# Kernel optimization log

Hardware: AMD Instinct MI355X
Metric: run time of the kernel (lower is better)

Reference implementation:

```python
import jax, jax.numpy as jnp
import numpy as np

K = 5            # kernel_size per dim
KD = K ** 3      # 125 spline weight slots
DIM = 3
NUM_GRAPHS = 64
# (n_nodes, n_edges, c_in, c_mid, c_out) per pyramid level
LEVELS = [(20000, 320000, 1, 32, 64), (10000, 160000, 1, 64, 64),
          (5000, 80000, 1, 64, 64), (2500, 40000, 1, 64, 64), (1250, 20000, 1, 64, 64)]


def setup_inputs() -> dict:
    key = jax.random.key(0)
    inp = {}
    for i, (n, e, cin, c1, c2) in enumerate(LEVELS, start=1):
        ks = jax.random.split(jax.random.fold_in(key, i), 8)
        inp[f'x{i}'] = jax.random.normal(ks[0], (n, cin), jnp.float32)
        inp[f'pseudo{i}'] = jax.random.uniform(ks[1], (e, DIM), jnp.float32)  # in [0,1)
        inp[f'edge_index{i}'] = jax.random.randint(ks[2], (2, e), 0, n)
        inp[f'batch{i}'] = jnp.sort(jax.random.randint(ks[3], (n,), 0, NUM_GRAPHS))
        inp[f'W{i}a'] = 0.1 * jax.random.normal(ks[4], (KD, cin, c1), jnp.float32)
        inp[f'root{i}a'] = 0.1 * jax.random.normal(ks[5], (cin, c1), jnp.float32)
        inp[f'bias{i}a'] = jnp.zeros((c1,), jnp.float32)
        inp[f'W{i}b'] = 0.1 * jax.random.normal(ks[6], (KD, c1, c2), jnp.float32)
        inp[f'root{i}b'] = 0.1 * jax.random.normal(ks[7], (c1, c2), jnp.float32)
        inp[f'bias{i}b'] = jnp.zeros((c2,), jnp.float32)
    kf = jax.random.fold_in(key, 99)
    inp['fc_w'] = 0.05 * jax.random.normal(kf, (5 * 64, 10), jnp.float32)
    inp['fc_b'] = jnp.zeros((10,), jnp.float32)
    return inp


def _spline_conv(x, src, dst, pseudo, W, Wroot, bias):
    """Degree-1 open B-spline conv (torch_spline_conv), mean aggregation + root weight."""
    n, cin = x.shape
    v = pseudo * (K - 1)                       # [E,3], pseudo in [0,1)
    k0 = jnp.floor(v).astype(jnp.int32)        # lower knot index per dim
    frac = v - k0                              # fractional part per dim
    xs = x[src]                                # [E,cin] gather source feats
    # accumulate basis-weighted source features per (target node, kernel slot)
    acc = jnp.zeros((n, KD, cin), x.dtype)
    for bits in range(2 ** DIM):               # 8 corner combinations of linear spline
        w = jnp.ones((src.shape[0],), x.dtype)
        idx = jnp.zeros((src.shape[0],), jnp.int32)
        for d in range(DIM):
            b = (bits >> d) & 1
            w = w * (frac[:, d] if b else 1.0 - frac[:, d])
            idx = idx * K + (k0[:, d] + b)
        acc = acc.at[dst, idx].add(w[:, None] * xs)
    deg = jnp.zeros((n,), x.dtype).at[dst].add(1.0)
    out = jnp.einsum('nki,kio->no', acc, W) / jnp.maximum(deg, 1.0)[:, None]
    return out + x @ Wroot + bias


def _readout(f, batch):
    s = jax.ops.segment_sum(f, batch, num_segments=NUM_GRAPHS)
    cnt = jax.ops.segment_sum(jnp.ones((f.shape[0],), f.dtype), batch, num_segments=NUM_GRAPHS)
    return s / jnp.maximum(cnt, 1.0)[:, None]   # scatter_mean


def _level(x, ei, ps, bt, Wa, ra, ba, Wb, rb, bb):
    f = jax.nn.relu(_spline_conv(x, ei[0], ei[1], ps, Wa, ra, ba))
    f = jax.nn.relu(_spline_conv(f, ei[0], ei[1], ps, Wb, rb, bb))
    return _readout(f, bt)


def reference(x1, pseudo1, edge_index1, batch1, W1a, root1a, bias1a, W1b, root1b, bias1b,
              x2, pseudo2, edge_index2, batch2, W2a, root2a, bias2a, W2b, root2b, bias2b,
              x3, pseudo3, edge_index3, batch3, W3a, root3a, bias3a, W3b, root3b, bias3b,
              x4, pseudo4, edge_index4, batch4, W4a, root4a, bias4a, W4b, root4b, bias4b,
              x5, pseudo5, edge_index5, batch5, W5a, root5a, bias5a, W5b, root5b, bias5b,
              fc_w, fc_b):
    levels = [
        (x1, edge_index1, pseudo1, batch1, W1a, root1a, bias1a, W1b, root1b, bias1b),
        (x2, edge_index2, pseudo2, batch2, W2a, root2a, bias2a, W2b, root2b, bias2b),
        (x3, edge_index3, pseudo3, batch3, W3a, root3a, bias3a, W3b, root3b, bias3b),
        (x4, edge_index4, pseudo4, batch4, W4a, root4a, bias4a, W4b, root4b, bias4b),
        (x5, edge_index5, pseudo5, batch5, W5a, root5a, bias5a, W5b, root5b, bias5b),
    ]
    res = [_level(*lv) for lv in levels]
    h = jnp.concatenate(res, axis=1)            # [B,320]; eval mode -> dropout is identity
    logits = h @ fc_w + fc_b                    # [B,10]
    return jax.nn.log_softmax(logits, axis=1)
```

## Files before the change

### kernel.cpp

```cpp
#include <hip/hip_runtime.h>
#include <hip/hip_fp16.h>
#include <math.h>

#define NUM_GRAPHS 64

typedef unsigned short ushortT;
typedef __attribute__((ext_vector_type(8))) short bf16x8;
typedef __attribute__((ext_vector_type(4))) float f32x4;

constexpr int cN[5]       = {20000, 10000, 5000, 2500, 1250};
constexpr int cE[5]       = {320000, 160000, 80000, 40000, 20000};
constexpr int cNOFF[6]    = {0, 20000, 30000, 35000, 37500, 38750};
constexpr int cEOFF[6]    = {0, 320000, 480000, 560000, 600000, 620000};
constexpr int cEBLKOFF[6] = {0, 1250, 1875, 2188, 2345, 2424};
constexpr int cNBLKOFF[6] = {0, 79, 119, 139, 149, 154};
constexpr int cMT[5]      = {5064, 2564, 1314, 689, 377};
constexpr int cTILEOFF[6] = {0, 5064, 7628, 8942, 9631, 10008};
constexpr int cSEOFF[6]   = {0, 324096, 488192, 572288, 616384, 640512};
constexpr int cF1OFF[6]   = {0, 640000, 1280000, 1600000, 1760000, 1840000};
constexpr int cWOFF[6]    = {0, 32000, 96000, 160000, 224000, 288000};
constexpr int cABLK[6]    = {0, 1250, 1875, 2188, 2345, 2424};
constexpr int cRBOFF[5]   = {0, 256, 768, 1280, 1792};
constexpr int cWAOFF[6]   = {0, 512, 1536, 2560, 3584, 4608};
constexpr int cRGB[6]     = {0, 313, 470, 549, 589, 609};
constexpr int cPAIR[6]    = {0, 2532, 3814, 4471, 4816, 5005};

struct P5f { const float* p[5]; };
struct P5i { const int* p[5]; };

__device__ __forceinline__ int lvl_e(int b) {
    return (b >= cEBLKOFF[4]) ? 4 : (b >= cEBLKOFF[3]) ? 3 : (b >= cEBLKOFF[2]) ? 2 : (b >= cEBLKOFF[1]) ? 1 : 0;
}
__device__ __forceinline__ int lvl_n(int b) {
    return (b >= cNBLKOFF[4]) ? 4 : (b >= cNBLKOFF[3]) ? 3 : (b >= cNBLKOFF[2]) ? 2 : (b >= cNBLKOFF[1]) ? 1 : 0;
}

__device__ __forceinline__ ushortT f2bf(float f) {
    union { float f; unsigned int u; } v; v.f = f;
    unsigned int r = (v.u + 0x7FFFu + ((v.u >> 16) & 1u)) >> 16;
    return (ushortT)r;
}
__device__ __forceinline__ float h2f_lo(unsigned int u) {
    return __half2float(__ushort_as_half((ushortT)(u & 0xFFFFu)));
}
__device__ __forceinline__ float h2f_hi(unsigned int u) {
    return __half2float(__ushort_as_half((ushortT)(u >> 16)));
}

__global__ void k_hist(P5f PS, P5i EI, int* __restrict__ dcnt, int* __restrict__ bb) {
    int b = blockIdx.x;
    int l = lvl_e(b);
    int lb = b - cEBLKOFF[l];
    int E = cE[l];
    __shared__ int h[64];
    int t = threadIdx.x;
    if (t < 64) h[t] = 0;
    __syncthreads();
    int e = lb * 256 + t;
    if (e < E) {
        atomicAdd(&dcnt[cNOFF[l] + EI.p[l][E + e]], 1);
        const float* ps = PS.p[l];
        int c = (int)floorf(ps[e * 3] * 4.f) * 16 + (int)floorf(ps[e * 3 + 1] * 4.f) * 4
              + (int)floorf(ps[e * 3 + 2] * 4.f);
        atomicAdd(&h[c], 1);
    }
    __syncthreads();
    if (t < 64) bb[(size_t)b * 64 + t] = h[t];
}

__global__ void k_cellscan(int* __restrict__ bb_all, int* __restrict__ csPad,
                           int* __restrict__ cellTot, int* __restrict__ cot_all) {
    int l = blockIdx.x;
    int c = threadIdx.x;
    int* bb = bb_all + (size_t)cEBLKOFF[l] * 64;
    int nblk = cEBLKOFF[l + 1] - cEBLKOFF[l];
    int run = 0;
    int b = 0;
    for (; b + 16 <= nblk; b += 16) {
        int v[16];
#pragma unroll
        for (int u = 0; u < 16; u++) v[u] = bb[(b + u) * 64 + c];
#pragma unroll
        for (int u = 0; u < 16; u++) { bb[(b + u) * 64 + c] = run; run += v[u]; }
    }
    for (; b < nblk; b++) { int v = bb[b * 64 + c]; bb[b * 64 + c] = run; run += v; }
    int tot = run;
    cellTot[l * 64 + c] = tot;
    int tiles = (tot + 63) >> 6;
    int x = tiles;
#pragma unroll
    for (int off = 1; off < 64; off <<= 1) { int y = __shfl_up(x, off, 64); if (c >= off) x += y; }
    int tileBase = x - tiles;
    csPad[l * 64 + c] = tileBase * 64;
    int* cot = cot_all + cTILEOFF[l];
    for (int i = 0; i < tiles; i++) {
        int vv = tot - (i << 6); if (vv > 64) vv = 64;
        cot[tileBase + i] = c | (vv << 8);
    }
    int nT = __shfl(x, 63, 64);
    int mt = cMT[l];
    for (int i = nT + c; i < mt; i += 64) cot[i] = -1;
}

__global__ void k_nscan1(const int* __restrict__ dcnt, int* __restrict__ dbase, int* __restrict__ bsum) {
    int b = blockIdx.x;
    int l = lvl_n(b);
    int lb = b - cNBLKOFF[l];
    int n = cN[l];
    __shared__ int sh[256];
    int t = threadIdx.x;
    int i = lb * 256 + t;
    int v = (i < n) ? dcnt[cNOFF[l] + i] : 0;
    sh[t] = v;
    __syncthreads();
    for (int off = 1; off < 256; off <<= 1) {
        int y = (t >= off) ? sh[t - off] : 0;
        __syncthreads();
        sh[t] += y;
        __syncthreads();
    }
    if (i < n) dbase[cNOFF[l] + i] = sh[t] - v;
    if (t == 255) bsum[b] = sh[255];
}

__global__ void k_nscan2(const int* __restrict__ bsum, int* __restrict__ boff) {
    int l = blockIdx.x;
    int o = cNBLKOFF[l];
    int nb = cNBLKOFF[l + 1] - o;
    int t = threadIdx.x;
    int v = (t < nb) ? bsum[o + t] : 0;
    int s = v;
#pragma unroll
    for (int off = 1; off < 64; off <<= 1) { int y = __shfl_up(s, off, 64); if (t >= off) s += y; }
    int tot = __shfl(s, 63, 64);
    if (t < nb) boff[o + t] = s - v;
    int t2 = t + 64;
    int v2 = (t2 < nb) ? bsum[o + t2] : 0;
    int s2 = v2;
#pragma unroll
    for (int off = 1; off < 64; off <<= 1) { int y = __shfl_up(s2, off, 64); if (t >= off) s2 += y; }
    if (t2 < nb) boff[o + t2] = tot + s2 - v2;
}

__global__ void k_scatter(P5f PS, P5i EI, const int* __restrict__ bb, const int* __restrict__ csPad,
                          const int* __restrict__ dbase, const int* __restrict__ boff,
                          int* __restrict__ rank,
                          int4* __restrict__ cbrec, int4* __restrict__ darec,
                          int* __restrict__ cpos) {
    int b = blockIdx.x;
    int l = lvl_e(b);
    int lb = b - cEBLKOFF[l];
    int E = cE[l];
    __shared__ int base[64];
    __shared__ int cnt[64];
    int t = threadIdx.x;
    if (t < 64) { base[t] = bb[(size_t)b * 64 + t] + csPad[l * 64 + t]; cnt[t] = 0; }
    __syncthreads();
    int e = lb * 256 + t;
    if (e >= E) return;
    const float* ps = PS.p[l];
    float v0 = ps[e * 3] * 4.f, v1 = ps[e * 3 + 1] * 4.f, v2 = ps[e * 3 + 2] * 4.f;
    float f0 = floorf(v0), f1v = floorf(v1), f2v = floorf(v2);
    int c = (int)f0 * 16 + (int)f1v * 4 + (int)f2v;
    int r = atomicAdd(&cnt[c], 1);
    int posc = base[c] + r;
    const int* ei = EI.p[l];
    int src = ei[e];
    int dst = ei[E + e];
    int posd = dbase[cNOFF[l] + dst] + boff[cNBLKOFF[l] + (dst >> 8)]
             + atomicAdd(&rank[cNOFF[l] + dst], 1);
    unsigned int fxfy = (unsigned int)__half_as_ushort(__float2half(v0 - f0))
                      | ((unsigned int)__half_as_ushort(__float2half(v1 - f1v)) << 16);
    unsigned int fzp  = (unsigned int)__half_as_ushort(__float2half(v2 - f2v));
    int4 rc;
    rc.x = src; rc.y = 0; rc.z = (int)fxfy; rc.w = (int)fzp;
    cbrec[cSEOFF[l] + posc] = rc;
    int4 rd;
    rd.x = src | (dst << 16); rd.y = c; rd.z = (int)fxfy; rd.w = (int)fzp;
    darec[cEOFF[l] + posd] = rd;
    cpos[cEOFF[l] + posd] = posc;
}

__global__ void k_wswz(P5f WB, P5f RootB, P5f WA,
                       uint4* __restrict__ hi4, uint4* __restrict__ rb, uint4* __restrict__ wa) {
    int idx = blockIdx.x * 256 + threadIdx.x;
    if (idx >= 294912) return;
    if (idx < 288000) {
        int l = (idx >= 224000) ? 4 : (idx >= 160000) ? 3 : (idx >= 96000) ? 2 : (idx >= 32000) ? 1 : 0;
        int local = idx - cWOFF[l];
        int T = l ? 2 : 1, C = l ? 64 : 32;
        int lane = local & 63;
        int blk = (local >> 6) & 3;
        int rest = local >> 8;
        int st = rest % T, s = rest / T;
        int q = lane >> 4, n = blk * 16 + (lane & 15);
        const float* W = WB.p[l];
        union { ushortT u[8]; uint4 v; } ph;
#pragma unroll
        for (int j = 0; j < 8; j++) {
            int k = st * 32 + q * 8 + j;
            ph.u[j] = f2bf(W[((size_t)s * C + k) * 64 + n]);
        }
        hi4[idx] = ph.v;
    } else if (idx < 290304) {
        int id2 = idx - 288000;
        int l = (id2 >= 1792) ? 4 : (id2 >= 1280) ? 3 : (id2 >= 768) ? 2 : (id2 >= 256) ? 1 : 0;
        int local = id2 - cRBOFF[l];
        int lane = local & 63;
        int w = (local >> 6) & 3;
        int st = local >> 8;
        int q = lane >> 4, n = w * 16 + (lane & 15);
        const float* R = RootB.p[l];
        union { ushortT u[8]; uint4 v; } ph;
#pragma unroll
        for (int j = 0; j < 8; j++) {
            int k = st * 32 + q * 8 + j;
            ph.u[j] = f2bf(R[k * 64 + n]);
        }
        rb[id2] = ph.v;
    } else {
        int id3 = idx - 290304;
        int l = (id3 >= cWAOFF[4]) ? 4 : (id3 >= cWAOFF[3]) ? 3 : (id3 >= cWAOFF[2]) ? 2 : (id3 >= cWAOFF[1]) ? 1 : 0;
        int local = id3 - cWAOFF[l];
        int C1 = l ? 64 : 32;
        int numN = C1 / 16;
        int lane = local & 63;
        int rest = local >> 6;
        int nb = rest % numN, st = rest / numN;
        int q = lane >> 4, n = nb * 16 + (lane & 15);
        const float* Wsrc = WA.p[l];
        union { ushortT u[8]; uint4 v; } ph;
#pragma unroll
        for (int j = 0; j < 8; j++) {
            int k = st * 32 + q * 8 + j;
            ph.u[j] = (k < 125) ? f2bf(Wsrc[k * C1 + n]) : (ushortT)0;
        }
        wa[id3] = ph.v;
    }
}

__launch_bounds__(256)
__global__ void conv_a_fused(P5f X, P5f RootA, P5f BiasA,
                             const int4* __restrict__ darec, const uint4* __restrict__ wasw,
                             const int* __restrict__ dbase, const int* __restrict__ boff,
                             const int* __restrict__ dcnt, ushortT* __restrict__ f1bf) {
    __shared__ float S[16 * 126];
    __shared__ ushortT Sbf[16 * 136];
    __shared__ int infoS[256];
    __shared__ unsigned int fxyS[256];
    __shared__ unsigned int fzS[256];
    __shared__ float xsS[256];
    int b = blockIdx.x;
    int l = (b >= cABLK[4]) ? 4 : (b >= cABLK[3]) ? 3 : (b >= cABLK[2]) ? 2 : (b >= cABLK[1]) ? 1 : 0;
    int node0 = (b - cABLK[l]) * 16;
    int n = cN[l];
    int nn = n - node0; if (nn > 16) nn = 16;
    int t = threadIdx.x;
    for (int i = t; i < 16 * 126; i += 256) S[i] = 0.f;
    const int* db = dbase + cNOFF[l];
    const int* bo = boff + cNBLKOFF[l];
    int estart = db[node0] + bo[node0 >> 8];
    int vend = node0 + nn;
    int eend = (vend >= n) ? cE[l] : (db[vend] + bo[vend >> 8]);
    const float* x = X.p[l];
    const int4* dr = darec + cEOFF[l];
    const int bx = t & 1, by = (t >> 1) & 1, bz = (t >> 2) & 1;
    for (int cs = estart; cs < eend; cs += 256) {
        int p = cs + t;
        if (p < eend) {
            int4 r = dr[p];
            infoS[t] = ((((unsigned int)r.x) >> 16) - node0) * 64 + r.y;
            fxyS[t] = (unsigned int)r.z;
            fzS[t] = (unsigned int)r.w;
            xsS[t] = x[r.x & 0xFFFF];
        }
        __syncthreads();
        int ne = eend - cs; if (ne > 256) ne = 256;
        for (int j = (t >> 3); j < ne; j += 32) {
            int info = infoS[j];
            int nl = info >> 6, cell = info & 63;
            unsigned int uz = fxyS[j];
            float fx = h2f_lo(uz), fy = h2f_hi(uz), fz = h2f_lo(fzS[j]);
            float xs = xsS[j];
            int cx = cell >> 4, cy = (cell >> 2) & 3, cz = cell & 3;
            int slot = (cx + bx) * 25 + (cy + by) * 5 + (cz + bz);
            float wc = (bx ? fx : 1.f - fx) * (by ? fy : 1.f - fy) * (bz ? fz : 1.f - fz);
            atomicAdd(&S[nl * 126 + slot], wc * xs);
        }
        __syncthreads();
    }
    for (int i = t; i < 16 * 128; i += 256) {
        int node = i >> 7, k = i & 127;
        float v = (k < 126) ? S[node * 126 + k] : 0.f;
        Sbf[node * 136 + k] = f2bf(v);
    }
    __syncthreads();
    int lane = t & 63, w = t >> 6;
    int C1 = l ? 64 : 32;
    int numN = C1 >> 4;
    if (w < numN) {
        int q = lane >> 4, m = lane & 15;
        const uint4* wl = wasw + cWAOFF[l];
        f32x4 acc = (f32x4){0.f, 0.f, 0.f, 0.f};
#pragma unroll
        for (int st = 0; st < 4; st++) {
            bf16x8 a = *(const bf16x8*)&Sbf[m * 136 + st * 32 + q * 8];
            bf16x8 bw = __builtin_bit_cast(bf16x8, wl[(st * numN + w) * 64 + lane]);
            acc = __builtin_amdgcn_mfma_f32_16x16x32_bf16(a, bw, acc, 0, 0, 0);
        }
        int ch = w * 16 + m;
        float rv = RootA.p[l][ch], bv = BiasA.p[l][ch];
        const int* dcl = dcnt + cNOFF[l];
        ushortT* f1bfl = f1bf + cF1OFF[l];
#pragma unroll
        for (int rr = 0; rr < 4; rr++) {
            int row = q * 4 + rr;
            if (row < nn) {
                int gnode = node0 + row;
                int dv = dcl[gnode];
                float d = (float)(dv > 1 ? dv : 1);
                float o = acc[rr] / d + x[gnode] * rv + bv;
                f1bfl[(size_t)gnode * C1 + ch] = f2bf(fmaxf(o, 0.f));
            }
        }
    }
}

__launch_bounds__(256)
__global__ void k_rgemm(const ushortT* __restrict__ f1bf, const uint4* __restrict__ rb,
                        float* __restrict__ f2) {
    int b = blockIdx.x;
    int l = (b >= cRGB[4]) ? 4 : (b >= cRGB[3]) ? 3 : (b >= cRGB[2]) ? 2 : (b >= cRGB[1]) ? 1 : 0;
    int node0 = (b - cRGB[l]) * 64;
    int n = cN[l];
    int nn = n - node0; if (nn > 64) nn = 64;
    int t = threadIdx.x;
    int lane = t & 63, w = t >> 6;
    int q = lane >> 4, m = lane & 15;
    const int CIN = l ? 64 : 32;
    const int T = l ? 2 : 1;
    const ushortT* fl = f1bf + cF1OFF[l];
    const uint4* rbl = rb + cRBOFF[l];
    f32x4 C[4];
#pragma unroll
    for (int mt = 0; mt < 4; mt++) C[mt] = (f32x4){0.f, 0.f, 0.f, 0.f};
    for (int st = 0; st < T; st++) {
        bf16x8 bh = __builtin_bit_cast(bf16x8, rbl[(st * 4 + w) * 64 + lane]);
#pragma unroll
        for (int mt = 0; mt < 4; mt++) {
            int row = 16 * mt + m;
            int nr = node0 + row; if (nr > n - 1) nr = n - 1;
            bf16x8 a = *(const bf16x8*)&fl[(size_t)nr * CIN + st * 32 + q * 8];
            C[mt] = __builtin_amdgcn_mfma_f32_16x16x32_bf16(a, bh, C[mt], 0, 0, 0);
        }
    }
#pragma unroll
    for (int mt = 0; mt < 4; mt++)
#pragma unroll
        for (int rr = 0; rr < 4; rr++) {
            int row = 16 * mt + q * 4 + rr;
            if (row < nn)
                f2[(size_t)(cNOFF[l] + node0 + row) * 64 + 16 * w + m] = C[mt][rr];
        }
}

template<int CIN>
__device__ __forceinline__ void stage_issue(const ushortT* __restrict__ f1bfl, int srcx,
                                            ushortT* lregion, int lane) {
    const int NC = CIN / 8;
#pragma unroll
    for (int i = 0; i < NC; i++) {
        int s = i * 64 + lane;
        int row = s / NC;
        int cp = s & (NC - 1);
        int chunk = cp ^ (row & (NC - 1));
        int src = __shfl(srcx, row, 64);
        const ushortT* gp = f1bfl + (size_t)src * CIN + chunk * 8;
        __builtin_amdgcn_global_load_lds(
            (const __attribute__((address_space(1))) void*)gp,
            (__attribute__((address_space(3))) void*)(lregion + (size_t)i * 512),
            16, 0, 0);
    }
}

template<int CIN>
__device__ __forceinline__ void read_ahr(const ushortT* st, bf16x8 (&ahr)[4][CIN / 32],
                                         int q, int m) {
    const int NC = CIN / 8;
#pragma unroll
    for (int mt = 0; mt < 4; mt++) {
        int row = 16 * mt + m;
#pragma unroll
        for (int s = 0; s < CIN / 32; s++) {
            int chunk = s * 4 + q;
            int cp = chunk ^ (row & (NC - 1));
            ahr[mt][s] = *(const bf16x8*)&st[(size_t)row * NC * 8 + cp * 8];
        }
    }
}

template<int CIN>
__device__ __forceinline__ void conv_b_tile_compute(
    const uint4* __restrict__ whiL, __half* __restrict__ pout,
    bf16x8 (&ahr)[4][CIN / 32], const float* __restrict__ wxy,
    const float* __restrict__ fzp, int cell, int tb, int lane, int wv) {
    const int T = CIN / 32;
    int q = lane >> 4, m = lane & 15;
    int cx = cell >> 4, cy = (cell >> 2) & 3, cz = cell & 3;
    float fzr[16];
#pragma unroll
    for (int mt = 0; mt < 4; mt++)
#pragma unroll
        for (int rr = 0; rr < 4; rr++)
            fzr[mt * 4 + rr] = fzp[16 * mt + q * 4 + rr];

    uint4 wb[2][2 * T];
    auto loadw = [&](int xy, uint4* dst) {
        int bx = xy & 1, by = xy >> 1;
        int s0 = (cx + bx) * 25 + (cy + by) * 5 + cz;
#pragma unroll
        for (int st = 0; st < T; st++) {
            dst[st]     = whiL[((size_t)(s0 * T + st) * 4 + wv) * 64 + lane];
            dst[T + st] = whiL[((size_t)((s0 + 1) * T + st) * 4 + wv) * 64 + lane];
        }
    };
    loadw(0, wb[0]);

    f32x4 acc[4];
#pragma unroll
    for (int mt = 0; mt < 4; mt++) acc[mt] = (f32x4){0.f, 0.f, 0.f, 0.f};

#pragma unroll
    for (int xy = 0; xy < 4; xy++) {
        uint4* cur = wb[xy & 1];
        if (xy < 3) loadw(xy + 1, wb[(xy + 1) & 1]);
        f32x4 C0[4], C1[4];
#pragma unroll
        for (int mt = 0; mt < 4; mt++) {
            C0[mt] = (f32x4){0.f, 0.f, 0.f, 0.f};
            C1[mt] = (f32x4){0.f, 0.f, 0.f, 0.f};
        }
#pragma unroll
        for (int st = 0; st < T; st++) {
            bf16x8 b0 = __builtin_bit_cast(bf16x8, cur[st]);
            bf16x8 b1 = __builtin_bit_cast(bf16x8, cur[T + st]);
#pragma unroll
            for (int mt = 0; mt < 4; mt++) {
                C0[mt] = __builtin_amdgcn_mfma_f32_16x16x32_bf16(ahr[mt][st], b0, C0[mt], 0, 0, 0);
                C1[mt] = __builtin_amdgcn_mfma_f32_16x16x32_bf16(ahr[mt][st], b1, C1[mt], 0, 0, 0);
            }
        }
        const float* wrow = &wxy[xy * 64];
#pragma unroll
        for (int mt = 0; mt < 4; mt++)
#pragma unroll
            for (int rr = 0; rr < 4; rr++) {
                float wxyv = wrow[16 * mt + q * 4 + rr];
                float dlt = C1[mt][rr] - C0[mt][rr];
                float tt = fmaf(fzr[mt * 4 + rr], dlt, C0[mt][rr]);
                acc[mt][rr] = fmaf(wxyv, tt, acc[mt][rr]);
            }
    }
#pragma unroll
    for (int mt = 0; mt < 4; mt++)
#pragma unroll
        for (int rr = 0; rr < 4; rr++) {
            int row = 16 * mt + q * 4 + rr;
            pout[(size_t)(tb + row) * 64 + 16 * wv + m] = __float2half(acc[mt][rr]);
        }
}

template<int CIN>
__device__ __forceinline__ void conv_b_pair(
    const ushortT* __restrict__ f1bfl, const int4* __restrict__ cbl,
    const uint4* __restrict__ whiL, __half* __restrict__ pout,
    int d0, int d1, int tb0, int tb1, int lane, int wv,
    ushortT* stage0, ushortT* stage1,
    float* __restrict__ wxy0, float* __restrict__ fz0,
    float* __restrict__ wxy1, float* __restrict__ fz1) {
    const int T = CIN / 32;
    const int NC = CIN / 8;
    int q = lane >> 4, m = lane & 15;
    bool has1 = d1 >= 0;
    int cell0 = d0 & 63, v0 = d0 >> 8;
    int cell1 = has1 ? (d1 & 63) : 0, v1 = has1 ? (d1 >> 8) : 0;

    int4 r0, r1;
    if (lane < v0) r0 = cbl[tb0 + lane]; else { r0.x = 0; r0.y = 0; r0.z = 0; r0.w = 0; }
    if (lane < v1) r1 = cbl[tb1 + lane]; else { r1.x = 0; r1.y = 0; r1.z = 0; r1.w = 0; }

    {
        unsigned int uz = (unsigned int)r0.z;
        float fx = h2f_lo(uz), fy = h2f_hi(uz);
        float gx = 1.f - fx, gy = 1.f - fy;
        wxy0[0 * 64 + lane] = gx * gy;
        wxy0[1 * 64 + lane] = fx * gy;
        wxy0[2 * 64 + lane] = gx * fy;
        wxy0[3 * 64 + lane] = fx * fy;
        fz0[lane] = h2f_lo((unsigned int)r0.w);
    }
    {
        unsigned int uz = (unsigned int)r1.z;
        float fx = h2f_lo(uz), fy = h2f_hi(uz);
        float gx = 1.f - fx, gy = 1.f - fy;
        wxy1[0 * 64 + lane] = gx * gy;
        wxy1[1 * 64 + lane] = fx * gy;
        wxy1[2 * 64 + lane] = gx * fy;
        wxy1[3 * 64 + lane] = fx * fy;
        fz1[lane] = h2f_lo((unsigned int)r1.w);
    }
    __builtin_amdgcn_wave_barrier();

    stage_issue<CIN>(f1bfl, r0.x, stage0, lane);
    if (has1) stage_issue<CIN>(f1bfl, r1.x, stage1, lane);

    if (has1) {
        if (CIN == 64) asm volatile("s_waitcnt vmcnt(8)" ::: "memory");
        else           asm volatile("s_waitcnt vmcnt(4)" ::: "memory");
    } else {
        asm volatile("s_waitcnt vmcnt(0)" ::: "memory");
    }

    bf16x8 ahr[4][T];
    read_ahr<CIN>(stage0, ahr, q, m);
    conv_b_tile_compute<CIN>(whiL, pout, ahr, wxy0, fz0, cell0, tb0, lane, wv);

    if (has1) {
        asm volatile("s_waitcnt vmcnt(0)" ::: "memory");
        read_ahr<CIN>(stage1, ahr, q, m);
        conv_b_tile_compute<CIN>(whiL, pout, ahr, wxy1, fz1, cell1, tb1, lane, wv);
    }
    (void)NC;
}

__launch_bounds__(256, 2)
__global__ void conv_b_all(const ushortT* __restrict__ f1bf, const int4* __restrict__ cbrec,
                           const uint4* __restrict__ whi, const int* __restrict__ cot,
                           __half* __restrict__ Ph) {
    __shared__ __align__(16) ushortT stageS[2][4096];
    __shared__ float wxyS[2][256];
    __shared__ float fzS[2][64];
    int t = threadIdx.x;
    int wv = t >> 6, lane = t & 63;
    int b = blockIdx.x;
    int l = (b >= cPAIR[4]) ? 4 : (b >= cPAIR[3]) ? 3 : (b >= cPAIR[2]) ? 2 : (b >= cPAIR[1]) ? 1 : 0;
    int p = b - cPAIR[l];
    int t0 = 2 * p, t1 = t0 + 1;
    const int* cotl = cot + cTILEOFF[l];
    int d0 = cotl[t0];
    int d1 = (t1 < cMT[l]) ? cotl[t1] : -1;
    if (d0 < 0) return;
    int tb0 = t0 * 64, tb1 = t1 * 64;
    if (l == 0)
        conv_b_pair<32>(f1bf, cbrec, whi, Ph, d0, d1, tb0, tb1, lane, wv,
                        stageS[0], stageS[1], wxyS[0], fzS[0], wxyS[1], fzS[1]);
    else
        conv_b_pair<64>(f1bf + cF1OFF[l], cbrec + cSEOFF[l], whi + cWOFF[l],
                        Ph + (size_t)cSEOFF[l] * 64, d0, d1, tb0, tb1, lane, wv,
                        stageS[0], stageS[1], wxyS[0], fzS[0], wxyS[1], fzS[1]);
}

__launch_bounds__(256)
__global__ void node_b_all(const __half* __restrict__ Ph, const int* __restrict__ cpos,
                           const int* __restrict__ dbase, const int* __restrict__ boff,
                           const int* __restrict__ dcnt, P5f BiasB, float* __restrict__ f2) {
    int lane = threadIdx.x & 63;
    int blk = blockIdx.x;
    int l, node;
    if (blk < 5000) {
        l = 0;
        node = blk * 4 + (threadIdx.x >> 6);
        if (node >= 20000) return;
    } else {
        const int NB2[4] = {0, 2500, 3750, 4375};
        int b2 = blk - 5000;
        int li = (b2 >= 4375) ? 3 : (b2 >= 3750) ? 2 : (b2 >= 2500) ? 1 : 0;
        l = li + 1;
        node = (b2 - NB2[li]) * 4 + (threadIdx.x >> 6);
        if (node >= cN[l]) return;
    }
    int start = dbase[cNOFF[l] + node] + boff[cNBLKOFF[l] + (node >> 8)];
    int deg = dcnt[cNOFF[l] + node];
    const __half* PhL = Ph + (size_t)cSEOFF[l] * 64;
    const int* cposL = cpos + cEOFF[l];
    float* f2row = f2 + (size_t)(cNOFF[l] + node) * 64;
    float s0 = 0.f, s1 = 0.f, s2 = 0.f, s3 = 0.f;
    int k = 0;
    for (; k + 4 <= deg; k += 4) {
        int r0 = cposL[start + k];
        int r1 = cposL[start + k + 1];
        int r2 = cposL[start + k + 2];
        int r3 = cposL[start + k + 3];
        s0 += __half2float(PhL[(size_t)r0 * 64 + lane]);
        s1 += __half2float(PhL[(size_t)r1 * 64 + lane]);
        s2 += __half2float(PhL[(size_t)r2 * 64 + lane]);
        s3 += __half2float(PhL[(size_t)r3 * 64 + lane]);
    }
    for (; k < deg; k++) s0 += __half2float(PhL[(size_t)cposL[start + k] * 64 + lane]);
    float s = (s0 + s1) + (s2 + s3);
    s /= (float)(deg > 1 ? deg : 1);
    s += f2row[lane] + BiasB.p[l][lane];
    f2row[lane] = fmaxf(s, 0.f);
}

__launch_bounds__(256)
__global__ void k_read(const float* __restrict__ f2, P5i Batch,
                       float* __restrict__ hsum, float* __restrict__ gcnt) {
    const int RC[5] = {0, 1250, 1875, 2188, 2345};
    int t = threadIdx.x;
    int lane = t & 63;
    int w = blockIdx.x * 4 + (t >> 6);
    if (w >= 2424) return;
    int l = (w >= 2345) ? 4 : (w >= 2188) ? 3 : (w >= 1875) ? 2 : (w >= 1250) ? 1 : 0;
    int base = (w - RC[l]) * 16;
    int Nl = cN[l];
    int nn = Nl - base; if (nn > 16) nn = 16;
    const int* batch = Batch.p[l];
    const float* fb = f2 + (size_t)(cNOFF[l] + base) * 64;
    int curg = -1; float hacc = 0.f; int crun = 0;
    for (int j = 0; j < nn; j++) {
        int g = batch[base + j];
        if (g != curg) {
            if (curg >= 0) {
                atomicAdd(&hsum[curg * 320 + l * 64 + lane], hacc);
                if (lane == 0) atomicAdd(&gcnt[l * 64 + curg], (float)crun);
            }
            curg = g; hacc = 0.f; crun = 0;
        }
        hacc += fb[(size_t)j * 64 + lane];
        crun++;
    }
    if (curg >= 0) {
        atomicAdd(&hsum[curg * 320 + l * 64 + lane], hacc);
        if (lane == 0) atomicAdd(&gcnt[l * 64 + curg], (float)crun);
    }
}

__global__ void fc_kernel(const float* __restrict__ hsum, const float* __restrict__ gcnt,
                          const float* __restrict__ fcw, const float* __restrict__ fcb,
                          float* __restrict__ out) {
    int g = blockIdx.x;
    int lane = threadIdx.x;
    float partial[10];
#pragma unroll
    for (int t = 0; t < 10; t++) partial[t] = 0.f;
#pragma unroll
    for (int k = 0; k < 5; k++) {
        int j = k * 64 + lane;
        float c = fmaxf(gcnt[k * 64 + g], 1.f);
        float h = hsum[g * 320 + j] / c;
        const float* fw = fcw + j * 10;
#pragma unroll
        for (int t = 0; t < 10; t++) partial[t] = fmaf(h, fw[t], partial[t]);
    }
#pragma unroll
    for (int off = 32; off >= 1; off >>= 1)
#pragma unroll
        for (int t = 0; t < 10; t++) partial[t] += __shfl_xor(partial[t], off, 64);
    if (lane == 0) {
        float logit[10];
#pragma unroll
        for (int t = 0; t < 10; t++) logit[t] = partial[t] + fcb[t];
        float m = logit[0];
#pragma unroll
        for (int t = 1; t < 10; t++) m = fmaxf(m, logit[t]);
        float sum = 0.f;
#pragma unroll
        for (int t = 0; t < 10; t++) sum += expf(logit[t] - m);
        float lse = m + logf(sum);
#pragma unroll
        for (int t = 0; t < 10; t++) out[g * 10 + t] = logit[t] - lse;
    }
}

extern "C" void kernel_launch(void* const* d_in, const int* in_sizes, int n_in,
                              void* d_out, int out_size, void* d_ws, size_t ws_size,
                              hipStream_t stream) {
    int* wsI = (int*)d_ws;
    int*   dcnt  = wsI;
    int*   rank  = dcnt + 38750;
    float* hsum  = (float*)(rank + 38750);
    float* gcnt  = hsum + 20480;
    float* f2    = gcnt + 320;
    int*   dbase = (int*)(f2 + 2480000);
    int*   bsum  = dbase + 38750;
    int*   boff  = bsum + 160;
    int*   cpos  = boff + 160;
    int*   bb    = cpos + 620000;
    int*   csPad = bb + 155136;
    int*   cellTot = csPad + 320;
    int*   cot   = cellTot + 320;
    int4*  cbrec = (int4*)(((size_t)(cot + 10008) + 15) & ~(size_t)15);
    int4*  darec = cbrec + 640512;
    ushortT* f1bf = (ushortT*)(darec + 620000);
    uint4* whi   = (uint4*)(((size_t)(f1bf + 1840000) + 15) & ~(size_t)15);
    uint4* rbsw  = whi + 288000;
    uint4* wasw  = rbsw + 2304;
    __half* Ph   = (__half*)(wasw + 4608);

    hipMemsetAsync(dcnt, 0, (size_t)(38750 * 2 + 20480 + 320) * sizeof(int), stream);

    P5f PS, X, WA, RootA, BiasA, WB, RootB, BiasB;
    P5i EI, Batch;
    for (int l = 0; l < 5; l++) {
        const int b = l * 10;
        X.p[l]     = (const float*)d_in[b + 0];
        PS.p[l]    = (const float*)d_in[b + 1];
        EI.p[l]    = (const int*)d_in[b + 2];
        Batch.p[l] = (const int*)d_in[b + 3];
        WA.p[l]    = (const float*)d_in[b + 4];
        RootA.p[l] = (const float*)d_in[b + 5];
        BiasA.p[l] = (const float*)d_in[b + 6];
        WB.p[l]    = (const float*)d_in[b + 7];
        RootB.p[l] = (const float*)d_in[b + 8];
        BiasB.p[l] = (const float*)d_in[b + 9];
    }

    k_hist<<<2424, 256, 0, stream>>>(PS, EI, dcnt, bb);
    k_cellscan<<<5, 64, 0, stream>>>(bb, csPad, cellTot, cot);
    k_nscan1<<<154, 256, 0, stream>>>(dcnt, dbase, bsum);
    k_nscan2<<<5, 64, 0, stream>>>(bsum, boff);
    k_scatter<<<2424, 256, 0, stream>>>(PS, EI, bb, csPad, dbase, boff, rank,
                                        cbrec, darec, cpos);
    k_wswz<<<1152, 256, 0, stream>>>(WB, RootB, WA, whi, rbsw, wasw);

    conv_a_fused<<<2424, 256, 0, stream>>>(X, RootA, BiasA, darec, wasw,
                                           dbase, boff, dcnt, f1bf);

    k_rgemm<<<609, 256, 0, stream>>>(f1bf, rbsw, f2);

    conv_b_all<<<5005, 256, 0, stream>>>(f1bf, cbrec, whi, cot, Ph);
    node_b_all<<<9688, 256, 0, stream>>>(Ph, cpos, dbase, boff, dcnt, BiasB, f2);

    k_read<<<606, 256, 0, stream>>>(f2, Batch, hsum, gcnt);
    fc_kernel<<<64, 64, 0, stream>>>(hsum, gcnt, (const float*)d_in[50], (const float*)d_in[51],
                                     (float*)d_out);
}
```

Measured before the change: 432.1 us.

## Process 32 nodes per conv_a block with prefetched edges and preloaded weight fragments

conv_a_fused now handles 32 destination nodes per block instead of 16, which halves the grid and lets all four waves run MFMA tasks rather than idling half of them. The bf16 staging buffer now aliases the fp32 accumulator through a register round-trip, and the weight fragments are loaded into registers at kernel start. Edge records and the source-feature gather for the next 256-edge chunk are prefetched into registers while the current chunk is being accumulated. The cost is more registers and fewer blocks, which could lower occupancy, and more edges per block could lengthen the serial atomic loop.

After: 433.3 us. Within noise of the previous version (+0.3%).

```diff
diff --git a/kernel.cpp b/kernel.cpp
--- a/kernel.cpp
+++ b/kernel.cpp
@@ -19,7 +19,7 @@
 constexpr int cSEOFF[6]   = {0, 324096, 488192, 572288, 616384, 640512};
 constexpr int cF1OFF[6]   = {0, 640000, 1280000, 1600000, 1760000, 1840000};
 constexpr int cWOFF[6]    = {0, 32000, 96000, 160000, 224000, 288000};
-constexpr int cABLK[6]    = {0, 1250, 1875, 2188, 2345, 2424};
+constexpr int cABLK32[6]  = {0, 625, 938, 1095, 1174, 1214};
 constexpr int cRBOFF[5]   = {0, 256, 768, 1280, 1792};
 constexpr int cWAOFF[6]   = {0, 512, 1536, 2560, 3584, 4608};
 constexpr int cRGB[6]     = {0, 313, 470, 549, 589, 609};
@@ -244,19 +244,34 @@
                              const int4* __restrict__ darec, const uint4* __restrict__ wasw,
                              const int* __restrict__ dbase, const int* __restrict__ boff,
                              const int* __restrict__ dcnt, ushortT* __restrict__ f1bf) {
-    __shared__ float S[16 * 126];
-    __shared__ ushortT Sbf[16 * 136];
+    __shared__ float S[32 * 126];
     __shared__ int infoS[256];
     __shared__ unsigned int fxyS[256];
     __shared__ unsigned int fzS[256];
     __shared__ float xsS[256];
     int b = blockIdx.x;
-    int l = (b >= cABLK[4]) ? 4 : (b >= cABLK[3]) ? 3 : (b >= cABLK[2]) ? 2 : (b >= cABLK[1]) ? 1 : 0;
-    int node0 = (b - cABLK[l]) * 16;
+    int l = (b >= cABLK32[4]) ? 4 : (b >= cABLK32[3]) ? 3 : (b >= cABLK32[2]) ? 2 : (b >= cABLK32[1]) ? 1 : 0;
+    int node0 = (b - cABLK32[l]) * 32;
     int n = cN[l];
-    int nn = n - node0; if (nn > 16) nn = 16;
+    int nn = n - node0; if (nn > 32) nn = 32;
     int t = threadIdx.x;
-    for (int i = t; i < 16 * 126; i += 256) S[i] = 0.f;
+    int lane = t & 63, wv = t >> 6;
+    int C1 = l ? 64 : 32;
+    int numN = C1 >> 4;
+    int nTask = 2 * numN;
+    const uint4* wl = wasw + cWAOFF[l];
+    uint4 wfrag0[4], wfrag1[4];
+    {
+        int w0 = wv % numN;
+#pragma unroll
+        for (int st = 0; st < 4; st++) wfrag0[st] = wl[(st * numN + w0) * 64 + lane];
+        if (nTask == 8) {
+            int w1 = wv;
+#pragma unroll
+            for (int st = 0; st < 4; st++) wfrag1[st] = wl[(st * numN + w1) * 64 + lane];
+        }
+    }
+    for (int i = t; i < 32 * 126; i += 256) S[i] = 0.f;
     const int* db = dbase + cNOFF[l];
     const int* bo = boff + cNBLKOFF[l];
     int estart = db[node0] + bo[node0 >> 8];
@@ -265,16 +280,18 @@
     const float* x = X.p[l];
     const int4* dr = darec + cEOFF[l];
     const int bx = t & 1, by = (t >> 1) & 1, bz = (t >> 2) & 1;
+    int4 rcur; float xcur;
+    if (estart + t < eend) { rcur = dr[estart + t]; xcur = x[rcur.x & 0xFFFF]; }
     for (int cs = estart; cs < eend; cs += 256) {
-        int p = cs + t;
-        if (p < eend) {
-            int4 r = dr[p];
-            infoS[t] = ((((unsigned int)r.x) >> 16) - node0) * 64 + r.y;
-            fxyS[t] = (unsigned int)r.z;
-            fzS[t] = (unsigned int)r.w;
-            xsS[t] = x[r.x & 0xFFFF];
+        if (cs + t < eend) {
+            infoS[t] = ((((unsigned int)rcur.x) >> 16) - node0) * 64 + rcur.y;
+            fxyS[t] = (unsigned int)rcur.z;
+            fzS[t] = (unsigned int)rcur.w;
+            xsS[t] = xcur;
         }
         __syncthreads();
+        int pn = cs + 256 + t;
+        if (pn < eend) { rcur = dr[pn]; xcur = x[rcur.x & 0xFFFF]; }
         int ne = eend - cs; if (ne > 256) ne = 256;
         for (int j = (t >> 3); j < ne; j += 32) {
             int info = infoS[j];
@@ -289,32 +306,39 @@
         }
         __syncthreads();
     }
-    for (int i = t; i < 16 * 128; i += 256) {
-        int node = i >> 7, k = i & 127;
-        float v = (k < 126) ? S[node * 126 + k] : 0.f;
-        Sbf[node * 136 + k] = f2bf(v);
+    ushortT* Sbf = (ushortT*)S;
+    float v[17];
+#pragma unroll
+    for (int j = 0; j < 17; j++) {
+        int i = t + 256 * j;
+        int node = i / 136, k = i % 136;
+        v[j] = (i < 4352 && k < 126) ? S[node * 126 + k] : 0.f;
     }
     __syncthreads();
-    int lane = t & 63, w = t >> 6;
-    int C1 = l ? 64 : 32;
-    int numN = C1 >> 4;
-    if (w < numN) {
-        int q = lane >> 4, m = lane & 15;
-        const uint4* wl = wasw + cWAOFF[l];
+#pragma unroll
+    for (int j = 0; j < 17; j++) {
+        int i = t + 256 * j;
+        if (i < 4352) Sbf[i] = f2bf(v[j]);
+    }
+    __syncthreads();
+    int q = lane >> 4, m = lane & 15;
+    const int* dcl = dcnt + cNOFF[l];
+    ushortT* f1bfl = f1bf + cF1OFF[l];
+    auto do_task = [&](int task, const uint4* wf) {
+        int g = task / numN;
+        int w = task - g * numN;
         f32x4 acc = (f32x4){0.f, 0.f, 0.f, 0.f};
 #pragma unroll
         for (int st = 0; st < 4; st++) {
-            bf16x8 a = *(const bf16x8*)&Sbf[m * 136 + st * 32 + q * 8];
-            bf16x8 bw = __builtin_bit_cast(bf16x8, wl[(st * numN + w) * 64 + lane]);
+            bf16x8 a = *(const bf16x8*)&Sbf[(16 * g + m) * 136 + st * 32 + q * 8];
+            bf16x8 bw = __builtin_bit_cast(bf16x8, wf[st]);
             acc = __builtin_amdgcn_mfma_f32_16x16x32_bf16(a, bw, acc, 0, 0, 0);
         }
         int ch = w * 16 + m;
         float rv = RootA.p[l][ch], bv = BiasA.p[l][ch];
-        const int* dcl = dcnt + cNOFF[l];
-        ushortT* f1bfl = f1bf + cF1OFF[l];
 #pragma unroll
         for (int rr = 0; rr < 4; rr++) {
-            int row = q * 4 + rr;
+            int row = 16 * g + q * 4 + rr;
             if (row < nn) {
                 int gnode = node0 + row;
                 int dv = dcl[gnode];
@@ -323,7 +347,9 @@
                 f1bfl[(size_t)gnode * C1 + ch] = f2bf(fmaxf(o, 0.f));
             }
         }
-    }
+    };
+    do_task(wv, wfrag0);
+    if (nTask == 8) do_task(wv + 4, wfrag1);
 }
 
 __launch_bounds__(256)
@@ -724,7 +750,7 @@
                                         cbrec, darec, cpos);
     k_wswz<<<1152, 256, 0, stream>>>(WB, RootB, WA, whi, rbsw, wasw);
 
-    conv_a_fused<<<2424, 256, 0, stream>>>(X, RootA, BiasA, darec, wasw,
+    conv_a_fused<<<1214, 256, 0, stream>>>(X, RootA, BiasA, darec, wasw,
                                            dbase, boff, dcnt, f1bf);
 
     k_rgemm<<<609, 256, 0, stream>>>(f1bf, rbsw, f2);
```
